# Kernel tuning notes

Hardware: AMD Instinct MI355X
Metric: run time of the kernel (lower is better)

Reference implementation:

```python
import jax, jax.numpy as jnp
import numpy as np

N, M, B = 8192, 64, 128
SEQ_W = 63
HID, OUT = 512, 256
SHIFT = (-1, 0, 1)
REPR = M + 1 + 1 + len(SHIFT) + 1  # 70


def setup_inputs() -> dict:
    key = jax.random.key(0)
    ks = jax.random.split(key, 16)
    rn = lambda k, shape, scale: jax.random.normal(k, shape, jnp.float32) * scale
    return {
        'x': rn(ks[0], (B, SEQ_W + 1), 1.0),
        'bank': rn(ks[1], (B, N, M), 1.0),
        'w_read_prev': jax.random.uniform(ks[2], (B, N), jnp.float32),
        'w_write_prev': jax.random.uniform(ks[3], (B, N), jnp.float32),
        'W0': rn(ks[4], (SEQ_W + 1, HID), (SEQ_W + 1) ** -0.5), 'b0': jnp.zeros((HID,), jnp.float32),
        'W1': rn(ks[5], (HID, HID), HID ** -0.5), 'b1': jnp.zeros((HID,), jnp.float32),
        'Wc': rn(ks[6], (HID, OUT), HID ** -0.5), 'bc': jnp.zeros((OUT,), jnp.float32),
        'Wr': rn(ks[7], (OUT, REPR), OUT ** -0.5), 'br': jnp.zeros((REPR,), jnp.float32),
        'Ww': rn(ks[8], (OUT, REPR), OUT ** -0.5), 'bw': jnp.zeros((REPR,), jnp.float32),
        'Wea': rn(ks[9], (2 * M, 2 * M), (2 * M) ** -0.5), 'bea': jnp.zeros((2 * M,), jnp.float32),
        'Wsp': rn(ks[10], (M, HID), M ** -0.5), 'bsp': jnp.zeros((HID,), jnp.float32),
        'Wo': rn(ks[11], (HID, SEQ_W), HID ** -0.5), 'bo': jnp.zeros((SEQ_W,), jnp.float32),
    }


def _split(rep):
    # rep: [B, REPR] -> k [B,M], beta [B,1], g [B,1], s [B,len(SHIFT)], gamma [B,1]
    return rep[:, :M], rep[:, M:M + 1], rep[:, M + 1:M + 2], rep[:, M + 2:-1], rep[:, -1:]


def _address(bank, w_prev, k, beta, g, s, gamma):
    # content addressing: cosine similarity between each memory row and key k
    dot = jnp.einsum('bnm,bm->bn', bank, k)                    # [B,N]
    denom = jnp.maximum(jnp.linalg.norm(bank, axis=2) *
                        jnp.linalg.norm(k, axis=1, keepdims=True), 1e-8)
    cos = dot / denom
    beta = jax.nn.relu(beta) + 1e-8
    wc = jax.nn.softmax(beta * cos, axis=1)                    # [B,N]
    g = jax.nn.sigmoid(g)
    wg = g * wc + (1.0 - g) * w_prev                           # interpolation
    s = jax.nn.softmax(s, axis=1)                              # [B,S]
    # circular shift, vectorized: ws[b,i] = sum_j s[b,j] * wg[b,(i+SHIFT[j]) mod N]
    idx = (jnp.arange(N)[:, None] + jnp.asarray(SHIFT)[None, :]) % N  # [N,S]
    ws = jnp.einsum('bns,bs->bn', wg[:, idx], s)
    gamma = jax.nn.relu(gamma) + 1.0
    wp = ws ** gamma                                           # sharpening
    return wp / wp.sum(axis=1, keepdims=True)


def _forward(x, bank, w_read_prev, w_write_prev, W0, b0, W1, b1, Wc, bc,
             Wr, br, Ww, bw, Wea, bea, Wsp, bsp, Wo, bo):
    lrelu = jax.nn.leaky_relu  # slope 0.01, matches F.leaky_relu default
    w_read_prev = w_read_prev / w_read_prev.sum(axis=1, keepdims=True)
    w_write_prev = w_write_prev / w_write_prev.sum(axis=1, keepdims=True)
    # FFController: n=2 hidden leaky_relu layers + output linear, then outer leaky_relu
    h = lrelu(x @ W0 + b0)
    h = lrelu(h @ W1 + b1)
    ctrl_out = lrelu(h @ Wc + bc)
    kr, betar, gr, sr, gammar = _split(ctrl_out @ Wr + br)
    kw, betaw, gw, sw, gammaw = _split(ctrl_out @ Ww + bw)
    mem_avg = bank.mean(axis=1)                                # [B,M]
    ea = jnp.concatenate([mem_avg, kw], axis=1) @ Wea + bea    # [B,2M]
    e = jax.nn.sigmoid(ea[:, :M])
    a = ea[:, M:]
    # write: address against OLD bank, then bank - w*e + w*a
    w_w = _address(bank, w_write_prev, kw, betaw, gw, sw, gammaw)
    new_bank = bank + w_w[:, :, None] * (a - e)[:, None, :]
    # read: address against UPDATED bank
    w_r = _address(new_bank, w_read_prev, kr, betar, gr, sr, gammar)
    out = jnp.einsum('bnm,bn->bm', new_bank, w_r)              # [B,M]
    seq = lrelu(out @ Wsp + bsp)
    return jax.nn.sigmoid(seq @ Wo + bo)                       # [B,SEQ_W]


def reference(x, bank, w_read_prev, w_write_prev, W0, b0, W1, b1, Wc, bc,
              Wr, br, Ww, bw, Wea, bea, Wsp, bsp, Wo, bo):
    return _forward(x, bank, w_read_prev, w_write_prev, W0, b0, W1, b1, Wc, bc,
                    Wr, br, Ww, bw, Wea, bea, Wsp, bsp, Wo, bo)
```

## Files before the change

### kernel.cpp

```cpp
#include <hip/hip_runtime.h>
#include <hip/hip_fp16.h>
#include <math.h>

#define NN 8192
#define MM 64
#define BB 128
#define HIDC 512
#define OUTC 256
#define SEQW 63

#define CHUNKS 64
#define CH2    32

#define OFF_KR    0
#define OFF_KW    8192
#define OFF_PR    16384
#define OFF_PW    17408
#define OFF_BS    18432
#define OFF_D     19456
#define OFF_PMSUM 27648
#define OFF_POUT  551936
#define OFF_DOTW  814080
#define OFF_DOTR  1862656
#define OFF_RN2   2911232
#define OFF_DOTD  3959808
#define OFF_WW    5008384
#define OFF_WR    6056960
#define OFF_HB    8388608

__device__ __forceinline__ float lrelu(float x){ return x > 0.f ? x : 0.01f*x; }
__device__ __forceinline__ float sigm(float x){ return 1.f/(1.f+__expf(-x)); }

typedef float fx4 __attribute__((ext_vector_type(4)));
__device__ __forceinline__ float4 ntload4(const float* p){
  fx4 v = __builtin_nontemporal_load((const fx4*)p);
  return make_float4(v.x, v.y, v.z, v.w);
}

__device__ __forceinline__ float2 h2f(unsigned u){
  __half2 h = *reinterpret_cast<__half2*>(&u);
  return __half22float2(h);
}

__device__ float block_reduce_sum(float v, float* red) {
  for (int m = 32; m >= 1; m >>= 1) v += __shfl_xor(v, m);
  int wid = threadIdx.x >> 6;
  int nw = (blockDim.x + 63) >> 6;
  if ((threadIdx.x & 63) == 0) red[wid] = v;
  __syncthreads();
  if (threadIdx.x == 0) { float s = 0.f; for (int i = 0; i < nw; ++i) s += red[i]; red[0] = s; }
  __syncthreads();
  float r = red[0];
  __syncthreads();
  return r;
}

__device__ float2 block_reduce_sum2(float2 v, float* red) {
  for (int m = 32; m >= 1; m >>= 1) { v.x += __shfl_xor(v.x, m); v.y += __shfl_xor(v.y, m); }
  int wid = threadIdx.x >> 6;
  int nw = (blockDim.x + 63) >> 6;
  if ((threadIdx.x & 63) == 0) { red[wid] = v.x; red[16 + wid] = v.y; }
  __syncthreads();
  if (threadIdx.x == 0) {
    float sx = 0.f, sy = 0.f;
    for (int i = 0; i < nw; ++i) { sx += red[i]; sy += red[16 + i]; }
    red[0] = sx; red[16] = sy;
  }
  __syncthreads();
  float2 r = make_float2(red[0], red[16]);
  __syncthreads();
  return r;
}

__global__ __launch_bounds__(512) void ctrl_kernel(
    const float* __restrict__ x,
    const float* __restrict__ W0, const float* __restrict__ b0,
    const float* __restrict__ W1, const float* __restrict__ b1,
    const float* __restrict__ Wc, const float* __restrict__ bc,
    const float* __restrict__ Wr, const float* __restrict__ br,
    const float* __restrict__ Ww, const float* __restrict__ bw,
    float* __restrict__ ws)
{
  int b = blockIdx.x, t = threadIdx.x;
  __shared__ float xs[64];
  __shared__ float h0[512];
  __shared__ float h1[512];
  __shared__ float ct[256];
  __shared__ float rr[70], rw[70];
  if (t < 64) xs[t] = x[b*64 + t];
  __syncthreads();
  float acc = b0[t];
  for (int i = 0; i < 64; ++i) acc += xs[i] * W0[i*HIDC + t];
  h0[t] = lrelu(acc);
  __syncthreads();
  acc = b1[t];
  for (int i = 0; i < 512; ++i) acc += h0[i] * W1[i*HIDC + t];
  h1[t] = lrelu(acc);
  __syncthreads();
  if (t < 256) {
    acc = bc[t];
    for (int i = 0; i < 512; ++i) acc += h1[i] * Wc[i*OUTC + t];
    ct[t] = lrelu(acc);
  }
  __syncthreads();
  if (t < 70) {
    float ar = br[t], aw = bw[t];
    for (int i = 0; i < 256; ++i) { float c = ct[i]; ar += c * Wr[i*70 + t]; aw += c * Ww[i*70 + t]; }
    rr[t] = ar; rw[t] = aw;
  }
  __syncthreads();
  if (t < 64) { ws[OFF_KR + b*64 + t] = rr[t]; ws[OFF_KW + b*64 + t] = rw[t]; }
  if (t == 0) {
    float* p = ws + OFF_PR + b*8;
    p[0] = fmaxf(rr[64], 0.f) + 1e-8f;
    p[1] = sigm(rr[65]);
    float m = fmaxf(rr[66], fmaxf(rr[67], rr[68]));
    float e0 = expf(rr[66]-m), e1 = expf(rr[67]-m), e2 = expf(rr[68]-m);
    float ss = e0+e1+e2;
    p[2] = e0/ss; p[3] = e1/ss; p[4] = e2/ss;
    p[5] = fmaxf(rr[69], 0.f) + 1.f;
    float n2 = 0.f; for (int i = 0; i < 64; ++i) n2 += rr[i]*rr[i];
    p[6] = sqrtf(n2);
  }
  if (t == 1) {
    float* p = ws + OFF_PW + b*8;
    p[0] = fmaxf(rw[64], 0.f) + 1e-8f;
    p[1] = sigm(rw[65]);
    float m = fmaxf(rw[66], fmaxf(rw[67], rw[68]));
    float e0 = expf(rw[66]-m), e1 = expf(rw[67]-m), e2 = expf(rw[68]-m);
    float ss = e0+e1+e2;
    p[2] = e0/ss; p[3] = e1/ss; p[4] = e2/ss;
    p[5] = fmaxf(rw[69], 0.f) + 1.f;
    float n2 = 0.f; for (int i = 0; i < 64; ++i) n2 += rw[i]*rw[i];
    p[6] = sqrtf(n2);
  }
}

__global__ __launch_bounds__(256, 4) void bank_pass1(const float* __restrict__ bank,
                                                     float* __restrict__ ws,
                                                     ushort* __restrict__ hbank)
{
  int blk = blockIdx.x;
  int b  = blk >> 6;
  int ch = blk & 63;
  int n0 = ch << 7;
  int t = threadIdx.x;
  int cg = t & 15;
  int rl = t >> 4;
  __shared__ float kwS[64], krS[64], msum[64];
  if (t < 64) { kwS[t] = ws[OFF_KW + b*64 + t]; krS[t] = ws[OFF_KR + b*64 + t]; msum[t] = 0.f; }
  __syncthreads();
  float4 kw4 = *(float4*)&kwS[cg*4];
  float4 kr4 = *(float4*)&krS[cg*4];

  float4 v[8];
  #pragma unroll
  for (int it = 0; it < 8; ++it) {
    int n = n0 + rl + it*16;
    v[it] = ntload4(&bank[((size_t)b*NN + n)*MM + cg*4]);
  }
  #pragma unroll
  for (int it = 0; it < 8; ++it) {
    int n = n0 + rl + it*16;
    __half2 ha = __floats2half2_rn(v[it].x, v[it].y);
    __half2 hb = __floats2half2_rn(v[it].z, v[it].w);
    uint2 hw;
    hw.x = *reinterpret_cast<unsigned*>(&ha);
    hw.y = *reinterpret_cast<unsigned*>(&hb);
    *(uint2*)&hbank[((size_t)b*NN + n)*MM + cg*4] = hw;
  }
  float dw[8], dr[8], r2[8];
  float m0=0.f, m1=0.f, m2=0.f, m3=0.f;
  #pragma unroll
  for (int it = 0; it < 8; ++it) {
    dw[it] = v[it].x*kw4.x + v[it].y*kw4.y + v[it].z*kw4.z + v[it].w*kw4.w;
    dr[it] = v[it].x*kr4.x + v[it].y*kr4.y + v[it].z*kr4.z + v[it].w*kr4.w;
    r2[it] = v[it].x*v[it].x + v[it].y*v[it].y + v[it].z*v[it].z + v[it].w*v[it].w;
    m0 += v[it].x; m1 += v[it].y; m2 += v[it].z; m3 += v[it].w;
  }
  #pragma unroll
  for (int m = 1; m < 16; m <<= 1) {
    #pragma unroll
    for (int it = 0; it < 8; ++it) {
      dw[it] += __shfl_xor(dw[it], m);
      dr[it] += __shfl_xor(dr[it], m);
      r2[it] += __shfl_xor(r2[it], m);
    }
  }
  if (cg == 0) {
    size_t base = (size_t)b*NN + n0 + rl;
    #pragma unroll
    for (int it = 0; it < 8; ++it) {
      ws[OFF_DOTW + base + it*16] = dw[it];
      ws[OFF_DOTR + base + it*16] = dr[it];
      ws[OFF_RN2  + base + it*16] = r2[it];
    }
  }
  atomicAdd(&msum[cg*4+0], m0);
  atomicAdd(&msum[cg*4+1], m1);
  atomicAdd(&msum[cg*4+2], m2);
  atomicAdd(&msum[cg*4+3], m3);
  __syncthreads();
  if (t < 64) ws[OFF_PMSUM + (size_t)(b*CHUNKS + ch)*64 + t] = msum[t];
}

__global__ __launch_bounds__(1024, 1) void address0(
    const float* __restrict__ wprev,
    const float* __restrict__ Wea, const float* __restrict__ bea,
    float* __restrict__ ws)
{
  int b = blockIdx.x, t = threadIdx.x;
  __shared__ float buf[NN];
  __shared__ float red[32];
  __shared__ float cat[128], eaS[128], dS[64];

  float wpr[8];
  float lps = 0.f;
  #pragma unroll
  for (int i = 0; i < 8; ++i) {
    wpr[i] = wprev[(size_t)b*NN + t + i*1024];
    lps += wpr[i];
  }

  if (t < 64) {
    float s = 0.f;
    for (int ch = 0; ch < CHUNKS; ++ch) s += ws[OFF_PMSUM + ((size_t)b*CHUNKS + ch)*64 + t];
    cat[t] = s * (1.0f/NN);
  } else if (t < 128) {
    cat[t] = ws[OFF_KW + b*64 + (t-64)];
  }
  __syncthreads();
  if (t < 128) {
    float acc = bea[t];
    for (int i = 0; i < 128; ++i) acc += cat[i] * Wea[i*128 + t];
    eaS[t] = acc;
  }
  __syncthreads();
  if (t < 64) {
    float dv = eaS[64+t] - sigm(eaS[t]);
    dS[t] = dv;
    ws[OFF_D + b*64 + t] = dv;
  }
  __syncthreads();
  if (t == 0) {
    float dd = 0.f, dk = 0.f;
    for (int i = 0; i < 64; ++i) { float dv = dS[i]; dd += dv*dv; dk += dv * ws[OFF_KR + b*64 + i]; }
    ws[OFF_BS + b*8 + 2] = dd;
    ws[OFF_BS + b*8 + 3] = dk;
  }

  const float* prm = ws + OFF_PW + b*8;
  float beta = prm[0], g = prm[1], s0 = prm[2], s1 = prm[3], s2 = prm[4], gamma = prm[5], knorm = prm[6];

  float lsum = 0.f;
  #pragma unroll
  for (int i = 0; i < 8; ++i) {
    int n = t + i*1024;
    size_t o = (size_t)b*NN + n;
    float c = ws[OFF_DOTW + o] / fmaxf(sqrtf(ws[OFF_RN2 + o]) * knorm, 1e-8f);
    float e = __expf(beta * (c - 1.f));
    buf[n] = e;
    lsum += e;
  }
  float2 se = block_reduce_sum2(make_float2(lps, lsum), red);
  float ie = g/se.y, ip = (1.f-g)/se.x;
  #pragma unroll
  for (int i = 0; i < 8; ++i) {
    int n = t + i*1024;
    buf[n] = buf[n]*ie + wpr[i]*ip;
  }
  __syncthreads();
  float l2 = 0.f;
  float wpv[8];
  #pragma unroll
  for (int i = 0; i < 8; ++i) {
    int n = t + i*1024;
    float wsv = s0*buf[(n + NN - 1) & (NN-1)] + s1*buf[n] + s2*buf[(n + 1) & (NN-1)];
    float p = exp2f(gamma * log2f(wsv));
    wpv[i] = p; l2 += p;
  }
  float wpsum = block_reduce_sum(l2, red);
  float invp = 1.f/wpsum;
  #pragma unroll
  for (int i = 0; i < 8; ++i)
    ws[OFF_WW + (size_t)b*NN + t + i*1024] = wpv[i]*invp;
}

__global__ __launch_bounds__(256, 4) void bank_pass2h(const ushort* __restrict__ hb, float* __restrict__ ws)
{
  int blk = blockIdx.x;
  int b  = (BB - 1) - (blk >> 5);
  int n0 = (blk & 31) << 8;
  int t = threadIdx.x;
  int cg = t & 7;
  int rl = t >> 3;
  __shared__ float dS[64];
  if (t < 64) dS[t] = ws[OFF_D + b*64 + t];
  __syncthreads();
  float d8[8];
  #pragma unroll
  for (int j = 0; j < 8; ++j) d8[j] = dS[cg*8 + j];

  uint4 hv[8];
  #pragma unroll
  for (int it = 0; it < 8; ++it) {
    int n = n0 + rl + it*32;
    hv[it] = *(const uint4*)&hb[((size_t)b*NN + n)*MM + cg*8];
  }
  float dd[8];
  #pragma unroll
  for (int it = 0; it < 8; ++it) {
    float2 f0 = h2f(hv[it].x), f1 = h2f(hv[it].y), f2 = h2f(hv[it].z), f3 = h2f(hv[it].w);
    dd[it] = f0.x*d8[0] + f0.y*d8[1] + f1.x*d8[2] + f1.y*d8[3]
           + f2.x*d8[4] + f2.y*d8[5] + f3.x*d8[6] + f3.y*d8[7];
  }
  #pragma unroll
  for (int m = 1; m < 8; m <<= 1) {
    #pragma unroll
    for (int it = 0; it < 8; ++it) dd[it] += __shfl_xor(dd[it], m);
  }
  if (cg == 0) {
    size_t base = (size_t)b*NN + n0 + rl;
    #pragma unroll
    for (int it = 0; it < 8; ++it) ws[OFF_DOTD + base + it*32] = dd[it];
  }
}

__global__ __launch_bounds__(1024, 1) void address1(
    const float* __restrict__ wprev, float* __restrict__ ws)
{
  int b = blockIdx.x, t = threadIdx.x;
  __shared__ float buf[NN];
  __shared__ float red[32];

  float wpr[8];
  float lps = 0.f;
  #pragma unroll
  for (int i = 0; i < 8; ++i) {
    wpr[i] = wprev[(size_t)b*NN + t + i*1024];
    lps += wpr[i];
  }

  const float* prm = ws + OFF_PR + b*8;
  float beta = prm[0], g = prm[1], s0 = prm[2], s1 = prm[3], s2 = prm[4], gamma = prm[5], knorm = prm[6];
  float dd2 = ws[OFF_BS + b*8 + 2], dkr = ws[OFF_BS + b*8 + 3];

  float lsum = 0.f;
  #pragma unroll
  for (int i = 0; i < 8; ++i) {
    int n = t + i*1024;
    size_t o = (size_t)b*NN + n;
    float wwv = ws[OFF_WW + o];
    float dot  = ws[OFF_DOTR + o] + wwv * dkr;
    float rn2v = fmaxf(ws[OFF_RN2 + o] + 2.f*wwv*ws[OFF_DOTD + o] + wwv*wwv*dd2, 0.f);
    float c = dot / fmaxf(sqrtf(rn2v) * knorm, 1e-8f);
    float e = __expf(beta * (c - 1.f));
    buf[n] = e;
    lsum += e;
  }
  float2 se = block_reduce_sum2(make_float2(lps, lsum), red);
  float ie = g/se.y, ip = (1.f-g)/se.x;
  #pragma unroll
  for (int i = 0; i < 8; ++i) {
    int n = t + i*1024;
    buf[n] = buf[n]*ie + wpr[i]*ip;
  }
  __syncthreads();
  float l2 = 0.f, lswr = 0.f;
  float wpv[8];
  #pragma unroll
  for (int i = 0; i < 8; ++i) {
    int n = t + i*1024;
    float wsv = s0*buf[(n + NN - 1) & (NN-1)] + s1*buf[n] + s2*buf[(n + 1) & (NN-1)];
    float p = exp2f(gamma * log2f(wsv));
    wpv[i] = p; l2 += p;
    lswr += p * ws[OFF_WW + (size_t)b*NN + n];
  }
  float2 ps = block_reduce_sum2(make_float2(l2, lswr), red);
  float invp = 1.f/ps.x;
  #pragma unroll
  for (int i = 0; i < 8; ++i)
    ws[OFF_WR + (size_t)b*NN + t + i*1024] = wpv[i]*invp;
  if (t == 0) ws[OFF_BS + b*8 + 4] = ps.y * invp;
}

__global__ __launch_bounds__(256, 4) void bank_pass3h(const ushort* __restrict__ hb, float* __restrict__ ws)
{
  int blk = blockIdx.x;
  int b  = blk >> 5;
  int ch = blk & 31;
  int n0 = ch << 8;
  int t = threadIdx.x;
  int cg = t & 7, rl = t >> 3;
  __shared__ float osum[64];
  if (t < 64) osum[t] = 0.f;
  __syncthreads();

  float wrv[8];
  #pragma unroll
  for (int it = 0; it < 8; ++it)
    wrv[it] = ws[OFF_WR + (size_t)b*NN + n0 + rl + it*32];
  uint4 hv[8];
  #pragma unroll
  for (int it = 0; it < 8; ++it) {
    int n = n0 + rl + it*32;
    hv[it] = *(const uint4*)&hb[((size_t)b*NN + n)*MM + cg*8];
  }
  float a[8];
  #pragma unroll
  for (int j = 0; j < 8; ++j) a[j] = 0.f;
  #pragma unroll
  for (int it = 0; it < 8; ++it) {
    float2 f0 = h2f(hv[it].x), f1 = h2f(hv[it].y), f2 = h2f(hv[it].z), f3 = h2f(hv[it].w);
    float w = wrv[it];
    a[0] += w*f0.x; a[1] += w*f0.y; a[2] += w*f1.x; a[3] += w*f1.y;
    a[4] += w*f2.x; a[5] += w*f2.y; a[6] += w*f3.x; a[7] += w*f3.y;
  }
  #pragma unroll
  for (int m = 8; m < 64; m <<= 1) {
    #pragma unroll
    for (int j = 0; j < 8; ++j) a[j] += __shfl_xor(a[j], m);
  }
  if ((t & 56) == 0) {
    #pragma unroll
    for (int j = 0; j < 8; ++j) atomicAdd(&osum[cg*8 + j], a[j]);
  }
  __syncthreads();
  if (t < 64) ws[OFF_POUT + (size_t)(b*CH2 + ch)*64 + t] = osum[t];
}

__global__ __launch_bounds__(512) void final_kernel(
    const float* __restrict__ Wsp, const float* __restrict__ bsp,
    const float* __restrict__ Wo,  const float* __restrict__ bo,
    float* __restrict__ out, float* __restrict__ ws)
{
  int b = blockIdx.x, t = threadIdx.x;
  __shared__ float o[64], seq[512];
  if (t < 64) {
    float s = 0.f;
    for (int ch = 0; ch < CH2; ++ch) s += ws[OFF_POUT + ((size_t)b*CH2 + ch)*64 + t];
    float swr = ws[OFF_BS + b*8 + 4];
    o[t] = s + swr * ws[OFF_D + b*64 + t];
  }
  __syncthreads();
  float acc = bsp[t];
  for (int i = 0; i < 64; ++i) acc += o[i] * Wsp[i*HIDC + t];
  seq[t] = lrelu(acc);
  __syncthreads();
  if (t < SEQW) {
    float a = bo[t];
    for (int i = 0; i < 512; ++i) a += seq[i] * Wo[i*SEQW + t];
    out[b*SEQW + t] = sigm(a);
  }
}

extern "C" void kernel_launch(void* const* d_in, const int* in_sizes, int n_in,
                              void* d_out, int out_size, void* d_ws, size_t ws_size,
                              hipStream_t stream) {
  const float* x    = (const float*)d_in[0];
  const float* bank = (const float*)d_in[1];
  const float* wrp  = (const float*)d_in[2];
  const float* wwp  = (const float*)d_in[3];
  const float* W0   = (const float*)d_in[4];
  const float* b0   = (const float*)d_in[5];
  const float* W1   = (const float*)d_in[6];
  const float* b1   = (const float*)d_in[7];
  const float* Wc   = (const float*)d_in[8];
  const float* bc   = (const float*)d_in[9];
  const float* Wr   = (const float*)d_in[10];
  const float* br   = (const float*)d_in[11];
  const float* Ww   = (const float*)d_in[12];
  const float* bw   = (const float*)d_in[13];
  const float* Wea  = (const float*)d_in[14];
  const float* bea  = (const float*)d_in[15];
  const float* Wsp  = (const float*)d_in[16];
  const float* bsp  = (const float*)d_in[17];
  const float* Wo   = (const float*)d_in[18];
  const float* bo   = (const float*)d_in[19];
  float*  ws  = (float*)d_ws;
  ushort* hb  = (ushort*)(ws + OFF_HB);
  float*  out = (float*)d_out;

  ctrl_kernel<<<BB, 512, 0, stream>>>(x, W0,b0, W1,b1, Wc,bc, Wr,br, Ww,bw, ws);
  bank_pass1<<<BB*CHUNKS, 256, 0, stream>>>(bank, ws, hb);
  address0<<<BB, 1024, 0, stream>>>(wwp, Wea, bea, ws);
  bank_pass2h<<<BB*CH2, 256, 0, stream>>>(hb, ws);
  address1<<<BB, 1024, 0, stream>>>(wrp, ws);
  bank_pass3h<<<BB*CH2, 256, 0, stream>>>(hb, ws);
  final_kernel<<<BB, 512, 0, stream>>>(Wsp,bsp, Wo,bo, out, ws);
}
```

Measured before the change: 212.8 us.

## Software-pipeline batch halves across fused multi-role stage kernels

Splits the batch into two halves and merges kernels so each launch runs the per-batch addressing work for one half alongside the bank streaming pass for the other half. The serial 1024-thread addressing kernels, which leave the GPU underfilled, are meant to overlap with the bandwidth-heavy bank passes. Blocks also grow to 1024 threads, each covering more rows. The cost is one extra launch, and every block now reserves the large shared buffer even in the streaming role, which may reduce occupancy for the bank passes.

Measured after the change: 290.4 us. 36.5% more time.

```diff
diff --git a/kernel.cpp b/kernel.cpp
--- a/kernel.cpp
+++ b/kernel.cpp
@@ -9,8 +9,11 @@
 #define OUTC 256
 #define SEQW 63
 
-#define CHUNKS 64
-#define CH2    32
+#define GB   64
+#define P1C  16
+#define P2C  8
+#define P1B  (GB*P1C)
+#define P2B  (GB*P2C)
 
 #define OFF_KR    0
 #define OFF_KW    8192
@@ -45,10 +48,9 @@
 __device__ float block_reduce_sum(float v, float* red) {
   for (int m = 32; m >= 1; m >>= 1) v += __shfl_xor(v, m);
   int wid = threadIdx.x >> 6;
-  int nw = (blockDim.x + 63) >> 6;
   if ((threadIdx.x & 63) == 0) red[wid] = v;
   __syncthreads();
-  if (threadIdx.x == 0) { float s = 0.f; for (int i = 0; i < nw; ++i) s += red[i]; red[0] = s; }
+  if (threadIdx.x == 0) { float s = 0.f; for (int i = 0; i < 16; ++i) s += red[i]; red[0] = s; }
   __syncthreads();
   float r = red[0];
   __syncthreads();
@@ -58,12 +60,11 @@
 __device__ float2 block_reduce_sum2(float2 v, float* red) {
   for (int m = 32; m >= 1; m >>= 1) { v.x += __shfl_xor(v.x, m); v.y += __shfl_xor(v.y, m); }
   int wid = threadIdx.x >> 6;
-  int nw = (blockDim.x + 63) >> 6;
   if ((threadIdx.x & 63) == 0) { red[wid] = v.x; red[16 + wid] = v.y; }
   __syncthreads();
   if (threadIdx.x == 0) {
     float sx = 0.f, sy = 0.f;
-    for (int i = 0; i < nw; ++i) { sx += red[i]; sy += red[16 + i]; }
+    for (int i = 0; i < 16; ++i) { sx += red[i]; sy += red[16 + i]; }
     red[0] = sx; red[16] = sy;
   }
   __syncthreads();
@@ -136,32 +137,28 @@
   }
 }
 
-__global__ __launch_bounds__(256, 4) void bank_pass1(const float* __restrict__ bank,
-                                                     float* __restrict__ ws,
-                                                     ushort* __restrict__ hbank)
-{
-  int blk = blockIdx.x;
-  int b  = blk >> 6;
-  int ch = blk & 63;
-  int n0 = ch << 7;
-  int t = threadIdx.x;
+
+__device__ void role_p1(int b, int ch, int t, const float* __restrict__ bank,
+                        float* __restrict__ ws, ushort* __restrict__ hbank, float* sh)
+{
+  float* kwS = sh; float* krS = sh + 64; float* msum = sh + 128;
   int cg = t & 15;
   int rl = t >> 4;
-  __shared__ float kwS[64], krS[64], msum[64];
   if (t < 64) { kwS[t] = ws[OFF_KW + b*64 + t]; krS[t] = ws[OFF_KR + b*64 + t]; msum[t] = 0.f; }
   __syncthreads();
   float4 kw4 = *(float4*)&kwS[cg*4];
   float4 kr4 = *(float4*)&krS[cg*4];
+  int n0 = ch << 9;
 
   float4 v[8];
   #pragma unroll
   for (int it = 0; it < 8; ++it) {
-    int n = n0 + rl + it*16;
+    int n = n0 + rl + it*64;
     v[it] = ntload4(&bank[((size_t)b*NN + n)*MM + cg*4]);
   }
   #pragma unroll
   for (int it = 0; it < 8; ++it) {
-    int n = n0 + rl + it*16;
+    int n = n0 + rl + it*64;
     __half2 ha = __floats2half2_rn(v[it].x, v[it].y);
     __half2 hb = __floats2half2_rn(v[it].z, v[it].w);
     uint2 hw;
@@ -191,9 +188,9 @@
     size_t base = (size_t)b*NN + n0 + rl;
     #pragma unroll
     for (int it = 0; it < 8; ++it) {
-      ws[OFF_DOTW + base + it*16] = dw[it];
-      ws[OFF_DOTR + base + it*16] = dr[it];
-      ws[OFF_RN2  + base + it*16] = r2[it];
+      ws[OFF_DOTW + base + it*64] = dw[it];
+      ws[OFF_DOTR + base + it*64] = dr[it];
+      ws[OFF_RN2  + base + it*64] = r2[it];
     }
   }
   atomicAdd(&msum[cg*4+0], m0);
@@ -201,18 +198,15 @@
   atomicAdd(&msum[cg*4+2], m2);
   atomicAdd(&msum[cg*4+3], m3);
   __syncthreads();
-  if (t < 64) ws[OFF_PMSUM + (size_t)(b*CHUNKS + ch)*64 + t] = msum[t];
-}
-
-__global__ __launch_bounds__(1024, 1) void address0(
-    const float* __restrict__ wprev,
-    const float* __restrict__ Wea, const float* __restrict__ bea,
-    float* __restrict__ ws)
-{
-  int b = blockIdx.x, t = threadIdx.x;
-  __shared__ float buf[NN];
-  __shared__ float red[32];
-  __shared__ float cat[128], eaS[128], dS[64];
+  if (t < 64) ws[OFF_PMSUM + (size_t)(b*P1C + ch)*64 + t] = msum[t];
+}
+
+__device__ void role_addr0(int b, int t, const float* __restrict__ wprev,
+                           const float* __restrict__ Wea, const float* __restrict__ bea,
+                           float* __restrict__ ws, float* sh)
+{
+  float* buf = sh; float* red = sh + NN; float* cat = sh + NN + 32;
+  float* eaS = sh + NN + 160; float* dS = sh + NN + 288;
 
   float wpr[8];
   float lps = 0.f;
@@ -224,7 +218,7 @@
 
   if (t < 64) {
     float s = 0.f;
-    for (int ch = 0; ch < CHUNKS; ++ch) s += ws[OFF_PMSUM + ((size_t)b*CHUNKS + ch)*64 + t];
+    for (int ch = 0; ch < P1C; ++ch) s += ws[OFF_PMSUM + ((size_t)b*P1C + ch)*64 + t];
     cat[t] = s * (1.0f/NN);
   } else if (t < 128) {
     cat[t] = ws[OFF_KW + b*64 + (t-64)];
@@ -286,25 +280,23 @@
     ws[OFF_WW + (size_t)b*NN + t + i*1024] = wpv[i]*invp;
 }
 
-__global__ __launch_bounds__(256, 4) void bank_pass2h(const ushort* __restrict__ hb, float* __restrict__ ws)
-{
-  int blk = blockIdx.x;
-  int b  = (BB - 1) - (blk >> 5);
-  int n0 = (blk & 31) << 8;
-  int t = threadIdx.x;
+__device__ void role_p2h(int b, int ch, int t, const ushort* __restrict__ hb,
+                         float* __restrict__ ws, float* sh)
+{
+  float* dS = sh;
   int cg = t & 7;
   int rl = t >> 3;
-  __shared__ float dS[64];
   if (t < 64) dS[t] = ws[OFF_D + b*64 + t];
   __syncthreads();
   float d8[8];
   #pragma unroll
   for (int j = 0; j < 8; ++j) d8[j] = dS[cg*8 + j];
+  int n0 = ch << 10;
 
   uint4 hv[8];
   #pragma unroll
   for (int it = 0; it < 8; ++it) {
-    int n = n0 + rl + it*32;
+    int n = n0 + rl + it*128;
     hv[it] = *(const uint4*)&hb[((size_t)b*NN + n)*MM + cg*8];
   }
   float dd[8];
@@ -322,16 +314,14 @@
   if (cg == 0) {
     size_t base = (size_t)b*NN + n0 + rl;
     #pragma unroll
-    for (int it = 0; it < 8; ++it) ws[OFF_DOTD + base + it*32] = dd[it];
-  }
-}
-
-__global__ __launch_bounds__(1024, 1) void address1(
-    const float* __restrict__ wprev, float* __restrict__ ws)
-{
-  int b = blockIdx.x, t = threadIdx.x;
-  __shared__ float buf[NN];
-  __shared__ float red[32];
+    for (int it = 0; it < 8; ++it) ws[OFF_DOTD + base + it*128] = dd[it];
+  }
+}
+
+__device__ void role_addr1(int b, int t, const float* __restrict__ wprev,
+                           float* __restrict__ ws, float* sh)
+{
+  float* buf = sh; float* red = sh + NN;
 
   float wpr[8];
   float lps = 0.f;
@@ -384,26 +374,23 @@
   if (t == 0) ws[OFF_BS + b*8 + 4] = ps.y * invp;
 }
 
-__global__ __launch_bounds__(256, 4) void bank_pass3h(const ushort* __restrict__ hb, float* __restrict__ ws)
-{
-  int blk = blockIdx.x;
-  int b  = blk >> 5;
-  int ch = blk & 31;
-  int n0 = ch << 8;
-  int t = threadIdx.x;
+__device__ void role_p3h(int b, int ch, int t, const ushort* __restrict__ hb,
+                         float* __restrict__ ws, float* sh)
+{
+  float* osum = sh;
   int cg = t & 7, rl = t >> 3;
-  __shared__ float osum[64];
   if (t < 64) osum[t] = 0.f;
   __syncthreads();
+  int n0 = ch << 10;
 
   float wrv[8];
   #pragma unroll
   for (int it = 0; it < 8; ++it)
-    wrv[it] = ws[OFF_WR + (size_t)b*NN + n0 + rl + it*32];
+    wrv[it] = ws[OFF_WR + (size_t)b*NN + n0 + rl + it*128];
   uint4 hv[8];
   #pragma unroll
   for (int it = 0; it < 8; ++it) {
-    int n = n0 + rl + it*32;
+    int n = n0 + rl + it*128;
     hv[it] = *(const uint4*)&hb[((size_t)b*NN + n)*MM + cg*8];
   }
   float a[8];
@@ -426,32 +413,104 @@
     for (int j = 0; j < 8; ++j) atomicAdd(&osum[cg*8 + j], a[j]);
   }
   __syncthreads();
-  if (t < 64) ws[OFF_POUT + (size_t)(b*CH2 + ch)*64 + t] = osum[t];
-}
-
-__global__ __launch_bounds__(512) void final_kernel(
-    const float* __restrict__ Wsp, const float* __restrict__ bsp,
-    const float* __restrict__ Wo,  const float* __restrict__ bo,
-    float* __restrict__ out, float* __restrict__ ws)
-{
-  int b = blockIdx.x, t = threadIdx.x;
-  __shared__ float o[64], seq[512];
+  if (t < 64) ws[OFF_POUT + (size_t)(b*P2C + ch)*64 + t] = osum[t];
+}
+
+__device__ void role_final(int b, int t,
+                           const float* __restrict__ Wsp, const float* __restrict__ bsp,
+                           const float* __restrict__ Wo,  const float* __restrict__ bo,
+                           float* __restrict__ out, float* __restrict__ ws, float* sh)
+{
+  float* o = sh; float* seq = sh + 64;
   if (t < 64) {
     float s = 0.f;
-    for (int ch = 0; ch < CH2; ++ch) s += ws[OFF_POUT + ((size_t)b*CH2 + ch)*64 + t];
+    for (int ch = 0; ch < P2C; ++ch) s += ws[OFF_POUT + ((size_t)b*P2C + ch)*64 + t];
     float swr = ws[OFF_BS + b*8 + 4];
     o[t] = s + swr * ws[OFF_D + b*64 + t];
   }
   __syncthreads();
-  float acc = bsp[t];
-  for (int i = 0; i < 64; ++i) acc += o[i] * Wsp[i*HIDC + t];
-  seq[t] = lrelu(acc);
+  if (t < HIDC) {
+    float acc = bsp[t];
+    #pragma unroll 4
+    for (int i = 0; i < 64; ++i) acc += o[i] * Wsp[i*HIDC + t];
+    seq[t] = lrelu(acc);
+  }
   __syncthreads();
   if (t < SEQW) {
     float a = bo[t];
-    for (int i = 0; i < 512; ++i) a += seq[i] * Wo[i*SEQW + t];
+    for (int i = 0; i < HIDC; ++i) a += seq[i] * Wo[i*SEQW + t];
     out[b*SEQW + t] = sigm(a);
   }
+}
+
+
+__global__ __launch_bounds__(1024) void stage1(const float* __restrict__ bank,
+                                               float* __restrict__ ws, ushort* __restrict__ hb)
+{
+  __shared__ float sh[192];
+  int blk = blockIdx.x;
+  role_p1(blk >> 4, blk & 15, threadIdx.x, bank, ws, hb, sh);
+}
+
+__global__ __launch_bounds__(1024) void stage2(const float* __restrict__ bank,
+                                               const float* __restrict__ wwp,
+                                               const float* __restrict__ Wea, const float* __restrict__ bea,
+                                               float* __restrict__ ws, ushort* __restrict__ hb)
+{
+  __shared__ float sh[NN + 352];
+  int blk = blockIdx.x, t = threadIdx.x;
+  if (blk < GB) role_addr0(blk, t, wwp, Wea, bea, ws, sh);
+  else { int gb = blk - GB; role_p1(GB + (gb >> 4), gb & 15, t, bank, ws, hb, sh); }
+}
+
+__global__ __launch_bounds__(1024) void stage3(const ushort* __restrict__ hb,
+                                               const float* __restrict__ wwp,
+                                               const float* __restrict__ Wea, const float* __restrict__ bea,
+                                               float* __restrict__ ws)
+{
+  __shared__ float sh[NN + 352];
+  int blk = blockIdx.x, t = threadIdx.x;
+  if (blk < GB) role_addr0(GB + blk, t, wwp, Wea, bea, ws, sh);
+  else { int gb = blk - GB; role_p2h(gb >> 3, gb & 7, t, hb, ws, sh); }
+}
+
+__global__ __launch_bounds__(1024) void stage4(const ushort* __restrict__ hb,
+                                               const float* __restrict__ wrp,
+                                               float* __restrict__ ws)
+{
+  __shared__ float sh[NN + 352];
+  int blk = blockIdx.x, t = threadIdx.x;
+  if (blk < GB) role_addr1(blk, t, wrp, ws, sh);
+  else { int gb = blk - GB; role_p2h(GB + (gb >> 3), gb & 7, t, hb, ws, sh); }
+}
+
+__global__ __launch_bounds__(1024) void stage5(const ushort* __restrict__ hb,
+                                               const float* __restrict__ wrp,
+                                               float* __restrict__ ws)
+{
+  __shared__ float sh[NN + 352];
+  int blk = blockIdx.x, t = threadIdx.x;
+  if (blk < GB) role_addr1(GB + blk, t, wrp, ws, sh);
+  else { int gb = blk - GB; role_p3h(gb >> 3, gb & 7, t, hb, ws, sh); }
+}
+
+__global__ __launch_bounds__(1024) void stage6(const ushort* __restrict__ hb,
+                                               const float* __restrict__ Wsp, const float* __restrict__ bsp,
+                                               const float* __restrict__ Wo,  const float* __restrict__ bo,
+                                               float* __restrict__ out, float* __restrict__ ws)
+{
+  __shared__ float sh[NN + 352];
+  int blk = blockIdx.x, t = threadIdx.x;
+  if (blk < GB) role_final(blk, t, Wsp, bsp, Wo, bo, out, ws, sh);
+  else { int gb = blk - GB; role_p3h(GB + (gb >> 3), gb & 7, t, hb, ws, sh); }
+}
+
+__global__ __launch_bounds__(1024) void stage7(const float* __restrict__ Wsp, const float* __restrict__ bsp,
+                                               const float* __restrict__ Wo,  const float* __restrict__ bo,
+                                               float* __restrict__ out, float* __restrict__ ws)
+{
+  __shared__ float sh[576];
+  role_final(GB + blockIdx.x, threadIdx.x, Wsp, bsp, Wo, bo, out, ws, sh);
 }
 
 extern "C" void kernel_launch(void* const* d_in, const int* in_sizes, int n_in,
@@ -482,10 +541,11 @@
   float*  out = (float*)d_out;
 
   ctrl_kernel<<<BB, 512, 0, stream>>>(x, W0,b0, W1,b1, Wc,bc, Wr,br, Ww,bw, ws);
-  bank_pass1<<<BB*CHUNKS, 256, 0, stream>>>(bank, ws, hb);
-  address0<<<BB, 1024, 0, stream>>>(wwp, Wea, bea, ws);
-  bank_pass2h<<<BB*CH2, 256, 0, stream>>>(hb, ws);
-  address1<<<BB, 1024, 0, stream>>>(wrp, ws);
-  bank_pass3h<<<BB*CH2, 256, 0, stream>>>(hb, ws);
-  final_kernel<<<BB, 512, 0, stream>>>(Wsp,bsp, Wo,bo, out, ws);
-}
+  stage1<<<P1B,      1024, 0, stream>>>(bank, ws, hb);
+  stage2<<<GB + P1B, 1024, 0, stream>>>(bank, wwp, Wea, bea, ws, hb);
+  stage3<<<GB + P2B, 1024, 0, stream>>>(hb, wwp, Wea, bea, ws);
+  stage4<<<GB + P2B, 1024, 0, stream>>>(hb, wrp, ws);
+  stage5<<<GB + P2B, 1024, 0, stream>>>(hb, wrp, ws);
+  stage6<<<GB + P2B, 1024, 0, stream>>>(hb, Wsp, bsp, Wo, bo, out, ws);
+  stage7<<<GB,       1024, 0, stream>>>(Wsp, bsp, Wo, bo, out, ws);
+}
```
